# Kernel tuning notes

Measured on AMD Instinct MI355X. Metric: run time of the kernel, lower is better.

The kernel has to match this reference:

```python
import jax, jax.numpy as jnp
import numpy as np

IMG_H, IMG_W = 800, 1216
STRIDE = 16
SIZES = (128.0, 256.0, 512.0)
RATIOS = (0.5, 1.0, 2.0)
NMS_THRESH = 0.7
MIN_SIZE = 16.0
PRE_NMS = 6000   # testing mode
POST_NMS = 300   # testing mode


def _base_anchors():
    # torchvision-style: ratio = h/w, anchors centered at origin, xyxy
    base = []
    for s in SIZES:
        for r in RATIOS:
            hr = np.sqrt(r)
            w, h = s / hr, s * hr
            base.append([-w / 2.0, -h / 2.0, w / 2.0, h / 2.0])
    return jnp.asarray(np.array(base, dtype=np.float32))  # [A,4]


def _anchors(H, W):
    base = _base_anchors()                                  # [A,4]
    sx = jnp.arange(W, dtype=jnp.float32) * STRIDE
    sy = jnp.arange(H, dtype=jnp.float32) * STRIDE
    shift_x, shift_y = jnp.meshgrid(sx, sy)                 # [H,W] each
    shifts = jnp.stack([shift_x, shift_y, shift_x, shift_y], axis=-1)
    # row-major over (h, w), anchors innermost -> matches permute(0,2,3,1) layout
    return (shifts.reshape(-1, 1, 4) + base[None]).reshape(-1, 4)  # [H*W*A,4]


def _conv(x, w, b, pad):
    y = jax.lax.conv_general_dilated(x, w, (1, 1), pad,
                                     dimension_numbers=('NCHW', 'OIHW', 'NCHW'))
    return y + b[None, :, None, None]


def _decode(deltas, anchors):
    wa = anchors[:, 2] - anchors[:, 0]
    ha = anchors[:, 3] - anchors[:, 1]
    cxa = anchors[:, 0] + 0.5 * wa
    cya = anchors[:, 1] + 0.5 * ha
    cx = deltas[:, 0] * wa + cxa
    cy = deltas[:, 1] * ha + cya
    w = jnp.exp(deltas[:, 2]) * wa
    h = jnp.exp(deltas[:, 3]) * ha
    return jnp.stack([cx - 0.5 * w, cy - 0.5 * h, cx + 0.5 * w, cy + 0.5 * h], axis=-1)


def _nms(boxes, scores):
    # boxes: [N,4] sorted by descending score; greedy IoU-suppression NMS
    N = boxes.shape[0]
    areas = (boxes[:, 2] - boxes[:, 0]) * (boxes[:, 3] - boxes[:, 1])

    def body(i, st):
        sup, kidx, kval = st
        avail = jnp.where(sup, -jnp.inf, scores)
        j = jnp.argmax(avail)
        valid = avail[j] > -jnp.inf
        b = boxes[j]
        ix1 = jnp.maximum(b[0], boxes[:, 0])
        iy1 = jnp.maximum(b[1], boxes[:, 1])
        ix2 = jnp.minimum(b[2], boxes[:, 2])
        iy2 = jnp.minimum(b[3], boxes[:, 3])
        inter = jnp.clip(ix2 - ix1, 0.0) * jnp.clip(iy2 - iy1, 0.0)
        union = areas[j] + areas - inter
        iou = jnp.where(union > 0, inter / union, 0.0)
        sup2 = (sup | (iou > NMS_THRESH)).at[j].set(True)
        sup = jnp.where(valid, sup2, sup.at[j].set(True))
        return sup, kidx.at[i].set(j), kval.at[i].set(valid)

    sup0 = jnp.zeros((N,), jnp.bool_)
    _, kidx, kval = jax.lax.fori_loop(
        0, POST_NMS, body,
        (sup0, jnp.zeros((POST_NMS,), jnp.int32), jnp.zeros((POST_NMS,), jnp.bool_)))
    # fixed-size output [POST_NMS,4]; invalid slots zeroed
    return boxes[kidx] * kval[:, None].astype(boxes.dtype)


def setup_inputs() -> dict:
    key = jax.random.key(0)
    ks = jax.random.split(key, 4)
    return {
        'features': jax.random.normal(ks[0], (8, 512, 50, 76), jnp.float32),
        'conv_w': 0.01 * jax.random.normal(ks[1], (512, 512, 3, 3), jnp.float32),
        'conv_b': jnp.zeros((512,), jnp.float32),
        'cls_w': 0.01 * jax.random.normal(ks[2], (9, 512, 1, 1), jnp.float32),
        'cls_b': jnp.zeros((9,), jnp.float32),
        'box_w': 0.01 * jax.random.normal(ks[3], (36, 512, 1, 1), jnp.float32),
        'box_b': jnp.zeros((36,), jnp.float32),
    }


def reference(features, conv_w, conv_b, cls_w, cls_b, box_w, box_b):
    B, _, H, W = features.shape
    t = jax.nn.relu(_conv(features, conv_w, conv_b, 'SAME'))
    obj = _conv(t, cls_w, cls_b, 'VALID')                     # [B,A,H,W]
    objectness = jnp.transpose(obj, (0, 2, 3, 1)).reshape(B, -1)        # [B,N]
    bd = _conv(t, box_w, box_b, 'VALID')                      # [B,4A,H,W]
    bbox_deltas = jnp.transpose(bd, (0, 2, 3, 1)).reshape(B, -1, 4)     # [B,N,4]
    anchors = _anchors(H, W)                                  # [N,4]

    def per_image(scores, deltas):
        props = _decode(deltas, anchors)
        props = jnp.stack([jnp.clip(props[:, 0], 0.0, IMG_W),
                           jnp.clip(props[:, 1], 0.0, IMG_H),
                           jnp.clip(props[:, 2], 0.0, IMG_W),
                           jnp.clip(props[:, 3], 0.0, IMG_H)], axis=-1)
        keep = ((props[:, 2] - props[:, 0]) >= MIN_SIZE) & \
               ((props[:, 3] - props[:, 1]) >= MIN_SIZE)
        s = jnp.where(keep, scores, -jnp.inf)  # small boxes never selected
        top_s, top_i = jax.lax.top_k(s, PRE_NMS)
        return _nms(props[top_i], top_s)

    proposals = jax.vmap(per_image)(objectness, bbox_deltas)  # [B,POST_NMS,4]
    return proposals, objectness, bbox_deltas
```

## Files before the change

kernel.cpp:

```cpp
#include <hip/hip_runtime.h>
#include <stdint.h>
#include <math.h>

typedef unsigned int u32;
typedef unsigned long long u64;
typedef double d4 __attribute__((ext_vector_type(4)));
typedef _Float16 h8 __attribute__((ext_vector_type(8)));
typedef float f32x16 __attribute__((ext_vector_type(16)));

#define NPX    3800
#define NANCH  34200
#define NSEL   6000
#define NOUT   300
#define NPXP   4160

#define OFF_T        0ull
#define OFF_WTH      62259200ull
#define OFF_WTL      66977792ull
#define OFF_BOXES    71696384ull
#define OFF_ITEMS    76073984ull
#define OFF_FSPH     78262784ull
#define OFF_FSPL     112341504ull
#define WS_NEED_F16  146551296ull
#define OFF_PART     OFF_FSPH
#define WS_NEED_SPLITK (OFF_PART + 43776000ull)

#define GLL16(gsrc, ldst) \
    __builtin_amdgcn_global_load_lds((const __attribute__((address_space(1))) void*)(gsrc), \
                                     (__attribute__((address_space(3))) void*)(ldst), 16, 0, 0)

__global__ __launch_bounds__(256) void prep_kernel(const float* __restrict__ feat,
                                                   const float* __restrict__ cw,
                                                   _Float16* __restrict__ wh,
                                                   _Float16* __restrict__ wl,
                                                   _Float16* __restrict__ fh,
                                                   _Float16* __restrict__ fl) {
    const int bid = blockIdx.x;
    const int tid = threadIdx.x;

    if (bid < 9216) {
        int o = bid * 256 + tid;
        int ci = o & 511;
        int co = (o >> 9) & 511;
        int kk = o >> 18;
        float v = cw[(((co << 9) + ci) * 9) + kk] * 1024.0f;
        _Float16 h = (_Float16)v;
        float r = v - (float)h;
        wh[o] = h;
        wl[o] = (_Float16)r;
    } else if (bid < 9216 + 7680) {
        int idx = bid - 9216;
        const int pb = idx % 60; idx /= 60;
        const int b  = idx >> 4;
        const int ci0 = (idx & 15) << 5;
        const int p0  = pb << 6;
        const int px = tid >> 2, cg = tid & 3;
        const int p = p0 + px;
        if (p < NPX) {
            const int yy = p / 76, xx = p - yy * 76;
            h8 vh, vl;
            const float* sp = feat + ((size_t)(b * 512 + ci0 + (cg << 3))) * NPX + p;
            #pragma unroll
            for (int j = 0; j < 8; ++j) {
                float s = sp[(size_t)j * NPX] * 512.0f;
                _Float16 h = (_Float16)s;
                float rr = s - (float)h;
                vh[j] = h;
                vl[j] = (_Float16)rr;
            }
            const size_t dst = ((size_t)b * NPXP + (size_t)((yy + 1) * 80 + xx + 2)) * 512
                             + ci0 + (cg << 3);
            *(h8*)(fh + dst) = vh;
            *(h8*)(fl + dst) = vl;
        }
    } else {
        int idx = (bid - 16896) * 256 + tid;
        int task = idx >> 2, sub = idx & 3;
        if (task < 2880) {
            int b = task / 360, c = task - b * 360;
            int yp, xp;
            if      (c < 80)  { yp = 0;  xp = c; }
            else if (c < 160) { yp = 51; xp = c - 80; }
            else { int c2 = c - 160; yp = 1 + (c2 >> 2); int m = c2 & 3; xp = (m < 2) ? m : (76 + m); }
            const size_t base = ((size_t)b * NPXP + (size_t)(yp * 80 + xp)) * 512 + sub * 128;
            h8 z = {};
            #pragma unroll
            for (int j = 0; j < 16; ++j) {
                *(h8*)(fh + base + (j << 3)) = z;
                *(h8*)(fl + base + (j << 3)) = z;
            }
        }
    }
}

__global__ __launch_bounds__(512, 2) void conv3x3_f16_kernel(
    const _Float16* __restrict__ fh, const _Float16* __restrict__ fl,
    const _Float16* __restrict__ wh, const _Float16* __restrict__ wl,
    const float* __restrict__ bias, float* __restrict__ t)
{
    const int id  = blockIdx.x;
    const int b   = id & 7;
    const int g   = id >> 3;
    const int co0 = (g >> 4) << 7;
    const int pt0 = (g & 15) << 8;
    const int tid = threadIdx.x;
    const int w   = tid >> 6;
    const int l   = tid & 63;
    const int wm  = w >> 2, wn = w & 3;
    const int ln  = l & 31, lk = l >> 5;

    __shared__ __align__(16) _Float16 S[5][24][512];

    const _Float16* sb[3];
    u32 ldof[3];
    bool isA[3];
    const long long fbase = (long long)b * NPXP + pt0;
    #pragma unroll
    for (int i = 0; i < 3; ++i) {
        const int ti = w * 3 + i;
        ldof[i] = (u32)(ti * 1024 + l * 16);
        isA[i] = (ti < 8);
        if (ti < 8) {
            const int mt = ti >> 1, hl = ti & 1;
            sb[i] = (hl ? wl : wh) + ((long long)(co0 + (mt << 5) + ln) << 9) + (lk << 3);
        } else {
            const int tj = ti - 8, nt = tj >> 1, hl = tj & 1;
            sb[i] = (hl ? fl : fh) + ((fbase + (nt << 5) + ln) << 9) + (lk << 3);
        }
    }
    char* lbase = (char*)&S[0][0][0];

    auto stage = [&](int q, int slot) {
        const int kk  = q >> 5;
        const int ci0 = (q & 31) << 4;
        const long long offA = ((long long)kk << 18) + ci0;
        const int kd = (kk * 11) >> 5;
        const int s  = kd * 77 + kk - 81;
        const long long offB = ((long long)s << 9) + ci0;
        char* ld = lbase + slot * 24576;
        #pragma unroll
        for (int i = 0; i < 3; ++i) {
            const long long off = isA[i] ? offA : offB;
            GLL16(sb[i] + off, ld + ldof[i]);
        }
    };

    f32x16 acc[2][2], l2[2][2];
    #pragma unroll
    for (int i = 0; i < 2; ++i)
        #pragma unroll
        for (int j = 0; j < 2; ++j)
            #pragma unroll
            for (int gg = 0; gg < 16; ++gg) { acc[i][j][gg] = 0.0f; l2[i][j][gg] = 0.0f; }

    const int ao = l << 3;

    auto readFrags = [&](int slot, h8* Ah, h8* Al, h8* Bh, h8* Bl) {
        const _Float16* Sq = (const _Float16*)(lbase + slot * 24576);
        #pragma unroll
        for (int i = 0; i < 2; ++i) {
            const int mt = (wm << 1) + i, nt = (wn << 1) + i;
            Ah[i] = *(const h8*)(Sq + (((mt << 1) + 0) << 9) + ao);
            Al[i] = *(const h8*)(Sq + (((mt << 1) + 1) << 9) + ao);
            Bh[i] = *(const h8*)(Sq + ((8 + (nt << 1) + 0) << 9) + ao);
            Bl[i] = *(const h8*)(Sq + ((8 + (nt << 1) + 1) << 9) + ao);
        }
    };

    stage(0, 0); stage(1, 1); stage(2, 2);
    asm volatile("s_waitcnt vmcnt(3)" ::: "memory");
    __builtin_amdgcn_sched_barrier(0);
    __builtin_amdgcn_s_barrier();

    int s0 = 0;
    for (int F = 0; F < 144; ++F) {
        const int q0 = F << 1;
        int s1 = s0 + 1; if (s1 >= 5) s1 -= 5;
        int s3 = s0 + 3; if (s3 >= 5) s3 -= 5;
        int s4 = s0 + 4; if (s4 >= 5) s4 -= 5;
        if (q0 + 3 < 288) stage(q0 + 3, s3);
        if (q0 + 4 < 288) stage(q0 + 4, s4);

        h8 A0h[2], A0l[2], B0h[2], B0l[2];
        h8 A1h[2], A1l[2], B1h[2], B1l[2];
        readFrags(s0, A0h, A0l, B0h, B0l);
        __builtin_amdgcn_s_setprio(1);
        acc[0][0] = __builtin_amdgcn_mfma_f32_32x32x16_f16(A0h[0], B0h[0], acc[0][0], 0, 0, 0);
        acc[0][1] = __builtin_amdgcn_mfma_f32_32x32x16_f16(A0h[0], B0h[1], acc[0][1], 0, 0, 0);
        acc[1][0] = __builtin_amdgcn_mfma_f32_32x32x16_f16(A0h[1], B0h[0], acc[1][0], 0, 0, 0);
        acc[1][1] = __builtin_amdgcn_mfma_f32_32x32x16_f16(A0h[1], B0h[1], acc[1][1], 0, 0, 0);
        acc[0][0] = __builtin_amdgcn_mfma_f32_32x32x16_f16(A0h[0], B0l[0], acc[0][0], 0, 0, 0);
        acc[0][1] = __builtin_amdgcn_mfma_f32_32x32x16_f16(A0h[0], B0l[1], acc[0][1], 0, 0, 0);
        acc[1][0] = __builtin_amdgcn_mfma_f32_32x32x16_f16(A0h[1], B0l[0], acc[1][0], 0, 0, 0);
        acc[1][1] = __builtin_amdgcn_mfma_f32_32x32x16_f16(A0h[1], B0l[1], acc[1][1], 0, 0, 0);
        __builtin_amdgcn_s_setprio(0);
        readFrags(s1, A1h, A1l, B1h, B1l);
        __builtin_amdgcn_s_setprio(1);
        acc[0][0] = __builtin_amdgcn_mfma_f32_32x32x16_f16(A0l[0], B0h[0], acc[0][0], 0, 0, 0);
        acc[0][1] = __builtin_amdgcn_mfma_f32_32x32x16_f16(A0l[0], B0h[1], acc[0][1], 0, 0, 0);
        acc[1][0] = __builtin_amdgcn_mfma_f32_32x32x16_f16(A0l[1], B0h[0], acc[1][0], 0, 0, 0);
        acc[1][1] = __builtin_amdgcn_mfma_f32_32x32x16_f16(A0l[1], B0h[1], acc[1][1], 0, 0, 0);
        acc[0][0] = __builtin_amdgcn_mfma_f32_32x32x16_f16(A1h[0], B1h[0], acc[0][0], 0, 0, 0);
        acc[0][1] = __builtin_amdgcn_mfma_f32_32x32x16_f16(A1h[0], B1h[1], acc[0][1], 0, 0, 0);
        acc[1][0] = __builtin_amdgcn_mfma_f32_32x32x16_f16(A1h[1], B1h[0], acc[1][0], 0, 0, 0);
        acc[1][1] = __builtin_amdgcn_mfma_f32_32x32x16_f16(A1h[1], B1h[1], acc[1][1], 0, 0, 0);
        acc[0][0] = __builtin_amdgcn_mfma_f32_32x32x16_f16(A1h[0], B1l[0], acc[0][0], 0, 0, 0);
        acc[0][1] = __builtin_amdgcn_mfma_f32_32x32x16_f16(A1h[0], B1l[1], acc[0][1], 0, 0, 0);
        acc[1][0] = __builtin_amdgcn_mfma_f32_32x32x16_f16(A1h[1], B1l[0], acc[1][0], 0, 0, 0);
        acc[1][1] = __builtin_amdgcn_mfma_f32_32x32x16_f16(A1h[1], B1l[1], acc[1][1], 0, 0, 0);
        acc[0][0] = __builtin_amdgcn_mfma_f32_32x32x16_f16(A1l[0], B1h[0], acc[0][0], 0, 0, 0);
        acc[0][1] = __builtin_amdgcn_mfma_f32_32x32x16_f16(A1l[0], B1h[1], acc[0][1], 0, 0, 0);
        acc[1][0] = __builtin_amdgcn_mfma_f32_32x32x16_f16(A1l[1], B1h[0], acc[1][0], 0, 0, 0);
        acc[1][1] = __builtin_amdgcn_mfma_f32_32x32x16_f16(A1l[1], B1h[1], acc[1][1], 0, 0, 0);
        __builtin_amdgcn_s_setprio(0);

        if (((q0 + 1) & 7) == 7) {
            #pragma unroll
            for (int i = 0; i < 2; ++i)
                #pragma unroll
                for (int j = 0; j < 2; ++j) {
                    l2[i][j] += acc[i][j];
                    #pragma unroll
                    for (int gg = 0; gg < 16; ++gg) acc[i][j][gg] = 0.0f;
                }
        }

        if (F < 143) {
            if (q0 + 4 < 288) { asm volatile("s_waitcnt vmcnt(3)" ::: "memory"); }
            else              { asm volatile("s_waitcnt vmcnt(0)" ::: "memory"); }
            __builtin_amdgcn_sched_barrier(0);
            __builtin_amdgcn_s_barrier();
        }
        s0 += 2; if (s0 >= 5) s0 -= 5;
    }

    int rcp[16];
    {
        h8 pa, pb;
        #pragma unroll
        for (int j = 0; j < 8; ++j) { pa[j] = (_Float16)(float)ln; pb[j] = (_Float16)0.0625f; }
        f32x16 pr, pc;
        #pragma unroll
        for (int gg = 0; gg < 16; ++gg) { pr[gg] = 0.0f; pc[gg] = 0.0f; }
        pr = __builtin_amdgcn_mfma_f32_32x32x16_f16(pa, pb, pr, 0, 0, 0);
        pc = __builtin_amdgcn_mfma_f32_32x32x16_f16(pb, pa, pc, 0, 0, 0);
        #pragma unroll
        for (int gg = 0; gg < 16; ++gg)
            rcp[gg] = ((int)(pr[gg] + 0.5f)) | (((int)(pc[gg] + 0.5f)) << 8);
    }

    const double dsc = 1.0 / 524288.0;
    #pragma unroll
    for (int i = 0; i < 2; ++i) {
        #pragma unroll
        for (int j = 0; j < 2; ++j) {
            #pragma unroll
            for (int gg = 0; gg < 16; ++gg) {
                const int row = rcp[gg] & 255;
                const int col = rcp[gg] >> 8;
                const int co  = co0 + (wm << 6) + (i << 5) + row;
                const int pp  = pt0 + (wn << 6) + (j << 5) + col;
                const int yy  = pp / 80;
                const int xx  = pp - yy * 80;
                if (yy >= 1 && yy < 51 && xx >= 2 && xx < 78) {
                    const double v = (double)l2[i][j][gg] * dsc + (double)bias[co];
                    t[((size_t)(b * 512 + co)) * NPX + (yy - 1) * 76 + (xx - 2)]
                        = (float)(v > 0.0 ? v : 0.0);
                }
            }
        }
    }
}

__global__ __launch_bounds__(1024) void wtrans_kernel(const float* __restrict__ cw,
                                                      float* __restrict__ wt) {
    int o = blockIdx.x * 1024 + threadIdx.x;
    if (o >= 512*512*9) return;
    int co = o & 511;
    int ci = (o >> 9) & 511;
    int kk = o >> 18;
    wt[o] = cw[((co << 9) + ci) * 9 + kk];
}

__global__ __launch_bounds__(256, 2) void conv3x3_mfma_kernel(const float* __restrict__ feat,
                                                              const float* __restrict__ wt,
                                                              const float* __restrict__ bias,
                                                              float* __restrict__ t) {
    const int b   = blockIdx.z;
    const int co0 = blockIdx.y << 7;
    const int px0 = blockIdx.x << 6;
    const int tid = threadIdx.x;
    const int w    = tid >> 6;
    const int l    = tid & 63;
    const int quad = l >> 4;
    const int lc   = l & 15;

    __shared__ double BsF[2][1024];

    int rr[4], cc[4];
    {
        d4 pzr = {0.0, 0.0, 0.0, 0.0};
        d4 pzc = {0.0, 0.0, 0.0, 0.0};
        double paM = (double)lc;
        double pbN = (double)lc;
        pzr = __builtin_amdgcn_mfma_f64_16x16x4f64(paM, 1.0, pzr, 0, 0, 0);
        pzc = __builtin_amdgcn_mfma_f64_16x16x4f64(1.0, pbN, pzc, 0, 0, 0);
        #pragma unroll
        for (int g = 0; g < 4; ++g) {
            rr[g] = (((int)pzr[g]) >> 2) & 15;
            cc[g] = (((int)pzc[g]) >> 2) & 15;
        }
    }

    d4 acc[2][4];
    #pragma unroll
    for (int i = 0; i < 2; ++i)
        #pragma unroll
        for (int j = 0; j < 4; ++j) acc[i][j] = (d4){0.0, 0.0, 0.0, 0.0};

    const float* featb = feat + (size_t)b * 512 * NPX;

    const int b_quad = (tid >> 4) & 3;
    const int b_pxl  = ((tid >> 6) << 4) | (tid & 15);
    const int p      = px0 + b_pxl;
    const int py     = p / 76;
    const int px     = p - py * 76;
    const bool pvalid = (p < NPX);

    float vaf[8], vbf[4];
    double a_cur[8];

    auto loadA = [&](int q, float* va) {
        int kk  = q >> 5;
        int ci0 = (q & 31) << 4;
        const float* ap = wt + (((size_t)(kk * 512 + ci0 + quad)) << 9)
                             + co0 + (w << 5) + lc;
        #pragma unroll
        for (int ks = 0; ks < 4; ++ks) {
            va[ks * 2 + 0] = ap[(ks << 11)];
            va[ks * 2 + 1] = ap[(ks << 11) + 16];
        }
    };
    auto loadB = [&](int q, float* vb) {
        int kk  = q >> 5;
        int ci0 = (q & 31) << 4;
        int kd = kk / 3;
        int dy = kd - 1, dx = kk - kd * 3 - 1;
        int iy = py + dy, ix = px + dx;
        bool ok = pvalid && ((unsigned)iy < 50u) && ((unsigned)ix < 76u);
        if (ok) {
            const float* bp = featb + (size_t)(ci0 + b_quad) * NPX + iy * 76 + ix;
            #pragma unroll
            for (int j = 0; j < 4; ++j) vb[j] = bp[(size_t)(j << 2) * NPX];
        } else {
            vb[0] = vb[1] = vb[2] = vb[3] = 0.0f;
        }
    };

    loadA(0, vaf); loadB(0, vbf);
    #pragma unroll
    for (int j = 0; j < 4; ++j) BsF[0][tid + (j << 8)] = (double)vbf[j];
    #pragma unroll
    for (int j = 0; j < 8; ++j) a_cur[j] = (double)vaf[j];
    __syncthreads();

    for (int q = 0; q < 288; ++q) {
        const int cur = q & 1;
        if (q < 287) { loadA(q + 1, vaf); loadB(q + 1, vbf); }
        const double* bb = BsF[cur];
        #pragma unroll
        for (int ks = 0; ks < 4; ++ks) {
            const double* bp = bb + (ks << 8);
            double a0 = a_cur[ks * 2], a1 = a_cur[ks * 2 + 1];
            #pragma unroll
            for (int nt = 0; nt < 4; ++nt) {
                double bv = bp[(nt << 6) + l];
                acc[0][nt] = __builtin_amdgcn_mfma_f64_16x16x4f64(a0, bv, acc[0][nt], 0, 0, 0);
                acc[1][nt] = __builtin_amdgcn_mfma_f64_16x16x4f64(a1, bv, acc[1][nt], 0, 0, 0);
            }
        }
        if (q < 287) {
            #pragma unroll
            for (int j = 0; j < 4; ++j) BsF[cur ^ 1][tid + (j << 8)] = (double)vbf[j];
            #pragma unroll
            for (int j = 0; j < 8; ++j) a_cur[j] = (double)vaf[j];
            __syncthreads();
        }
    }

    #pragma unroll
    for (int mt = 0; mt < 2; ++mt) {
        #pragma unroll
        for (int g = 0; g < 4; ++g) {
            int co = co0 + (w << 5) + (mt << 4) + rr[g];
            double bs = (double)bias[co];
            float* row = t + ((size_t)b * 512 + co) * NPX;
            #pragma unroll
            for (int nt = 0; nt < 4; ++nt) {
                int pp = px0 + (nt << 4) + cc[g];
                if (pp < NPX) {
                    double v = acc[mt][nt][g] + bs;
                    row[pp] = (float)(v > 0.0 ? v : 0.0);
                }
            }
        }
    }
}

__global__ __launch_bounds__(64) void heads_partial_kernel(const float* __restrict__ t,
                                                           const float* __restrict__ cls_w,
                                                           const float* __restrict__ box_w,
                                                           double* __restrict__ part) {
    const int b = blockIdx.y, c = blockIdx.z;
    const int p = blockIdx.x * 64 + threadIdx.x;
    if (p >= NPX) return;
    const float* tb = t + ((size_t)b * 512 + c * 128) * NPX + p;

    double ac[9]  = {};
    double ab[36] = {};
    for (int ci = 0; ci < 128; ++ci) {
        double tv = (double)tb[(size_t)ci * NPX];
        int cw = c * 128 + ci;
        #pragma unroll
        for (int o = 0; o < 9;  ++o) ac[o] = fma((double)cls_w[o * 512 + cw], tv, ac[o]);
        #pragma unroll
        for (int o = 0; o < 36; ++o) ab[o] = fma((double)box_w[o * 512 + cw], tv, ab[o]);
    }
    double* dst = part + ((size_t)(c * 8 + b) * 45) * NPX + p;
    #pragma unroll
    for (int o = 0; o < 9;  ++o) dst[(size_t)o * NPX] = ac[o];
    #pragma unroll
    for (int o = 0; o < 36; ++o) dst[(size_t)(9 + o) * NPX] = ab[o];
}

__device__ __forceinline__ void decode_px(int b, int p, const double* s45,
                                          const float* cls_b, const float* box_b,
                                          float* out_obj, float* out_del,
                                          float* boxes, u64* items) {
    float* ob = out_obj + (size_t)b * NANCH + (size_t)p * 9;
    float* dl = out_del + (size_t)b * NANCH * 4 + (size_t)p * 36;
    const int yy = p / 76, xx = p - yy * 76;

    #pragma unroll
    for (int a = 0; a < 9; ++a) {
        double s  = s45[a] + (double)cls_b[a];
        ob[a] = (float)s;
        double d0 = s45[9 + 4*a + 0] + (double)box_b[4*a+0];
        double d1 = s45[9 + 4*a + 1] + (double)box_b[4*a+1];
        double d2 = s45[9 + 4*a + 2] + (double)box_b[4*a+2];
        double d3 = s45[9 + 4*a + 3] + (double)box_b[4*a+3];
        dl[4*a+0] = (float)d0; dl[4*a+1] = (float)d1;
        dl[4*a+2] = (float)d2; dl[4*a+3] = (float)d3;

        int si = a / 3, ri = a - si * 3;
        double sz = (si == 0) ? 128.0 : ((si == 1) ? 256.0 : 512.0);
        double hr = (ri == 0) ? 0.7071067811865476 : ((ri == 1) ? 1.0 : 1.4142135623730951);
        float bx2f = (float)(sz / hr * 0.5);
        float by2f = (float)(sz * hr * 0.5);

        double sx = (double)(xx * 16), sy = (double)(yy * 16);
        double x1 = sx - (double)bx2f, x2 = sx + (double)bx2f;
        double y1 = sy - (double)by2f, y2 = sy + (double)by2f;

        double wa = x2 - x1, ha = y2 - y1;
        double cxa = x1 + 0.5 * wa, cya = y1 + 0.5 * ha;
        double cx = d0 * wa + cxa, cy = d1 * ha + cya;
        double w  = exp(d2) * wa,  h  = exp(d3) * ha;

        double px1 = cx - 0.5 * w, py1 = cy - 0.5 * h;
        double px2 = cx + 0.5 * w, py2 = cy + 0.5 * h;
        px1 = fmin(fmax(px1, 0.0), 1216.0);
        py1 = fmin(fmax(py1, 0.0), 800.0);
        px2 = fmin(fmax(px2, 0.0), 1216.0);
        py2 = fmin(fmax(py2, 0.0), 800.0);

        bool keep = ((px2 - px1) >= 16.0) && ((py2 - py1) >= 16.0);
        double se = keep ? s : -INFINITY;

        u64 ubits = (u64)__double_as_longlong(se);
        u64 ka = (ubits >> 63) ? ~ubits : (ubits | 0x8000000000000000ull);
        u64 kd = ~ka;
        int n = p * 9 + a;
        items[(size_t)b * NANCH + n] = (kd & ~0xFFFFull) | (u64)(u32)n;
        *(float4*)(boxes + ((size_t)b * NANCH + n) * 4) =
            make_float4((float)px1, (float)py1, (float)px2, (float)py2);
    }
}

__global__ __launch_bounds__(64) void reduce_decode_kernel(const double* __restrict__ part,
                                                           const float* __restrict__ cls_b,
                                                           const float* __restrict__ box_b,
                                                           float* __restrict__ out_obj,
                                                           float* __restrict__ out_del,
                                                           float* __restrict__ boxes,
                                                           u64* __restrict__ items) {
    const int b = blockIdx.y;
    const int p = blockIdx.x * 64 + threadIdx.x;
    if (p >= NPX) return;
    double s45[45];
    #pragma unroll
    for (int o = 0; o < 45; ++o) {
        double s = part[((size_t)(0 * 8 + b) * 45 + o) * NPX + p];
        s += part[((size_t)(1 * 8 + b) * 45 + o) * NPX + p];
        s += part[((size_t)(2 * 8 + b) * 45 + o) * NPX + p];
        s += part[((size_t)(3 * 8 + b) * 45 + o) * NPX + p];
        s45[o] = s;
    }
    decode_px(b, p, s45, cls_b, box_b, out_obj, out_del, boxes, items);
}

__global__ __launch_bounds__(256) void heads_decode_kernel(const float* __restrict__ t,
                                                           const float* __restrict__ cls_w,
                                                           const float* __restrict__ cls_b,
                                                           const float* __restrict__ box_w,
                                                           const float* __restrict__ box_b,
                                                           float* __restrict__ out_obj,
                                                           float* __restrict__ out_del,
                                                           float* __restrict__ boxes,
                                                           u64* __restrict__ items) {
    const int b = blockIdx.y;
    const int p = blockIdx.x * 256 + threadIdx.x;
    if (p >= NPX) return;
    const float* tb = t + (size_t)b * 512 * NPX + p;
    double s45[45];
    #pragma unroll
    for (int o = 0; o < 45; ++o) s45[o] = 0.0;
    for (int ci = 0; ci < 512; ++ci) {
        double tv = (double)tb[(size_t)ci * NPX];
        #pragma unroll
        for (int o = 0; o < 9;  ++o) s45[o]     = fma((double)cls_w[o * 512 + ci], tv, s45[o]);
        #pragma unroll
        for (int o = 0; o < 36; ++o) s45[9 + o] = fma((double)box_w[o * 512 + ci], tv, s45[9 + o]);
    }
    decode_px(b, p, s45, cls_b, box_b, out_obj, out_del, boxes, items);
}

__device__ __forceinline__ bool iou_gt(float4 A, float4 B, float areaA, float areaB) {
    float ix1 = fmaxf(A.x, B.x), iy1 = fmaxf(A.y, B.y);
    float ix2 = fminf(A.z, B.z), iy2 = fminf(A.w, B.w);
    float iw = fmaxf(ix2 - ix1, 0.0f), ih = fmaxf(iy2 - iy1, 0.0f);
    float inter = iw * ih;
    float uni = areaA + areaB - inter;
    float iou = (uni > 0.0f) ? (inter / uni) : 0.0f;
    return iou > 0.7f;
}

__global__ __launch_bounds__(1024) void topk_nms_kernel(const u64* __restrict__ items,
                                                        const float* __restrict__ boxes,
                                                        float* __restrict__ out) {
    extern __shared__ u64 buf[];
    u32* hist = (u32*)buf;
    u32* scan = hist + 4096;
    u32* scal = hist + 5120;

    const int b   = blockIdx.x;
    const int tid = threadIdx.x;
    const u64* it = items + (size_t)b * NANCH;

    #pragma unroll
    for (int i = 0; i < 4; ++i) hist[tid * 4 + i] = 0;
    __syncthreads();
    for (int i = tid; i < NANCH; i += 1024)
        atomicAdd(&hist[(u32)(it[i] >> 52)], 1);
    __syncthreads();

    u32 B1, cum1;
    {
        u32 c0 = hist[tid*4], c1 = hist[tid*4+1], c2 = hist[tid*4+2], c3 = hist[tid*4+3];
        u32 S = c0 + c1 + c2 + c3;
        scan[tid] = S;
        __syncthreads();
        for (int off = 1; off < 1024; off <<= 1) {
            u32 v = (tid >= off) ? scan[tid - off] : 0;
            __syncthreads();
            scan[tid] += v;
            __syncthreads();
        }
        u32 excl = scan[tid] - S;
        const u32 target = 5999;
        if (target >= excl && target < excl + S) {
            u32 pfx = excl, bidx, cum;
            if      (target < pfx + c0)           { bidx = tid*4;   cum = pfx; }
            else if (target < pfx + c0 + c1)      { bidx = tid*4+1; cum = pfx + c0; }
            else if (target < pfx + c0 + c1 + c2) { bidx = tid*4+2; cum = pfx + c0 + c1; }
            else                                  { bidx = tid*4+3; cum = pfx + c0 + c1 + c2; }
            scal[0] = bidx; scal[1] = cum;
        }
    }
    __syncthreads();
    B1 = scal[0]; cum1 = scal[1];
    __syncthreads();

    #pragma unroll
    for (int i = 0; i < 4; ++i) hist[tid * 4 + i] = 0;
    __syncthreads();
    for (int i = tid; i < NANCH; i += 1024) {
        u64 v = it[i];
        if ((u32)(v >> 52) == B1)
            atomicAdd(&hist[(u32)(v >> 40) & 0xFFF], 1);
    }
    __syncthreads();

    u32 B2;
    {
        u32 c0 = hist[tid*4], c1 = hist[tid*4+1], c2 = hist[tid*4+2], c3 = hist[tid*4+3];
        u32 S = c0 + c1 + c2 + c3;
        scan[tid] = S;
        __syncthreads();
        for (int off = 1; off < 1024; off <<= 1) {
            u32 v = (tid >= off) ? scan[tid - off] : 0;
            __syncthreads();
            scan[tid] += v;
            __syncthreads();
        }
        u32 excl = scan[tid] - S;
        const u32 target = 5999 - cum1;
        if (target >= excl && target < excl + S) {
            u32 pfx = excl, bidx;
            if      (target < pfx + c0)           bidx = tid*4;
            else if (target < pfx + c0 + c1)      bidx = tid*4+1;
            else if (target < pfx + c0 + c1 + c2) bidx = tid*4+2;
            else                                  bidx = tid*4+3;
            scal[2] = bidx;
        }
    }
    __syncthreads();
    B2 = scal[2];
    const u32 T = ((B1 << 12) | B2) + 1;
    __syncthreads();

    for (int i = tid; i < 8192; i += 1024) buf[i] = ~0ull;
    __syncthreads();
    u32* cnt = (u32*)&buf[8191];
    if (tid == 0) *cnt = 0;
    __syncthreads();
    for (int i = tid; i < NANCH; i += 1024) {
        u64 v = it[i];
        if ((u32)(v >> 40) < T) {
            u32 pos = atomicAdd(cnt, 1);
            if (pos < 8191) buf[pos] = v;
        }
    }
    __syncthreads();
    if (tid == 0) buf[8191] = ~0ull;
    __syncthreads();

    for (int size = 2; size <= 8192; size <<= 1) {
        for (int stride = size >> 1; stride > 0; stride >>= 1) {
            #pragma unroll
            for (int v = 0; v < 4; ++v) {
                int idx = tid + (v << 10);
                int i = 2 * idx - (idx & (stride - 1));
                int j = i + stride;
                bool up = ((i & size) == 0);
                u64 x = buf[i], y = buf[j];
                if ((x > y) == up) { buf[i] = y; buf[j] = x; }
            }
            __syncthreads();
        }
    }

    float4 bx6[6]; u32 dead6[6];
    #pragma unroll
    for (int s = 0; s < 6; ++s) {
        int r = tid + (s << 10);
        u64 v = buf[r];
        bool dd = (r >= NSEL) || ((u32)(v >> 32) >= 0xFFF00000u);
        float4 bb = make_float4(0.f, 0.f, 0.f, 0.f);
        if (!dd) {
            u32 n = (u32)(v & 0xFFFFull);
            bb = *(const float4*)(boxes + ((size_t)b * NANCH + n) * 4);
        }
        bx6[s] = bb;
        dead6[s] = dd ? 1u : 0u;
    }
    __syncthreads();

    float4* candbox = (float4*)buf;
    u64*    wmask   = (u64*)(buf + 2560);
    float4* accb    = (float4*)(buf + 3072);
    u32*    cntp    = (u32*)(buf + 3712);
    if (tid == 0) *cntp = 0;
    __syncthreads();

    for (int s = 0; s < 6; ++s) {
        int count = (int)*cntp;
        if (count >= NOUT) break;
        float4 mb = bx6[s];
        float  ma = (mb.z - mb.x) * (mb.w - mb.y);
        bool dd = dead6[s] != 0;
        for (int a2 = 0; a2 < count && !dd; ++a2) {
            float4 abx = accb[a2];
            if (iou_gt(mb, abx, ma, (abx.z - abx.x) * (abx.w - abx.y))) dd = true;
        }
        candbox[tid] = mb;
        u64 bal = __ballot(!dd);
        if ((tid & 63) == 0) wmask[tid >> 6] = bal;
        __syncthreads();
        if (tid < 64) {
            int cnt2 = count;
            for (int w2 = 0; w2 < 16 && cnt2 < NOUT; ++w2) {
                u64 mm = wmask[w2];
                while (mm != 0 && cnt2 < NOUT) {
                    int bit = __ffsll(mm) - 1;
                    mm &= (mm - 1);
                    float4 cb = candbox[(w2 << 6) + bit];
                    float  ca = (cb.z - cb.x) * (cb.w - cb.y);
                    bool okc = true;
                    for (int base = count; base < cnt2 && okc; base += 64) {
                        int idx = base + tid;
                        bool bad = false;
                        if (idx < cnt2) {
                            float4 abx = accb[idx];
                            bad = iou_gt(cb, abx, ca, (abx.z - abx.x) * (abx.w - abx.y));
                        }
                        if (__any(bad)) okc = false;
                    }
                    if (okc) {
                        if (tid == 0) accb[cnt2] = cb;
                        cnt2++;
                    }
                }
            }
            if (tid == 0) *cntp = (u32)cnt2;
        }
        __syncthreads();
    }

    int fin = (int)*cntp;
    for (int r = tid; r < NOUT; r += 1024) {
        float4 v = (r < fin) ? accb[r] : make_float4(0.f, 0.f, 0.f, 0.f);
        *(float4*)(out + ((size_t)b * NOUT + r) * 4) = v;
    }
}

extern "C" void kernel_launch(void* const* d_in, const int* in_sizes, int n_in,
                              void* d_out, int out_size, void* d_ws, size_t ws_size,
                              hipStream_t stream) {
    const float* feat   = (const float*)d_in[0];
    const float* conv_w = (const float*)d_in[1];
    const float* conv_b = (const float*)d_in[2];
    const float* cls_w  = (const float*)d_in[3];
    const float* cls_b  = (const float*)d_in[4];
    const float* box_w  = (const float*)d_in[5];
    const float* box_b  = (const float*)d_in[6];

    float* out       = (float*)d_out;
    float* out_props = out;
    float* out_obj   = out + 9600;
    float* out_del   = out + 9600 + 273600;

    char* ws = (char*)d_ws;
    float*    t     = (float*)(ws + OFF_T);
    _Float16* wth   = (_Float16*)(ws + OFF_WTH);
    _Float16* wtl   = (_Float16*)(ws + OFF_WTL);
    float*    wtf   = (float*)(ws + OFF_WTH);
    float*    boxes = (float*)(ws + OFF_BOXES);
    u64*      items = (u64*)(ws + OFF_ITEMS);
    _Float16* fsph  = (_Float16*)(ws + OFF_FSPH);
    _Float16* fspl  = (_Float16*)(ws + OFF_FSPL);
    double*   part  = (double*)(ws + OFF_PART);

    if (ws_size >= WS_NEED_F16) {
        hipLaunchKernelGGL(prep_kernel, dim3(16941), dim3(256), 0, stream,
                           feat, conv_w, wth, wtl, fsph, fspl);
        hipLaunchKernelGGL(conv3x3_f16_kernel, dim3(512), dim3(512), 0, stream,
                           fsph, fspl, wth, wtl, conv_b, t);
    } else {
        hipLaunchKernelGGL(wtrans_kernel, dim3(2304), dim3(1024), 0, stream, conv_w, wtf);
        hipLaunchKernelGGL(conv3x3_mfma_kernel, dim3(60, 4, 8), dim3(256), 0, stream,
                           feat, wtf, conv_b, t);
    }
    if (ws_size >= WS_NEED_SPLITK) {
        hipLaunchKernelGGL(heads_partial_kernel, dim3(60, 8, 4), dim3(64), 0, stream,
                           t, cls_w, box_w, part);
        hipLaunchKernelGGL(reduce_decode_kernel, dim3(60, 8), dim3(64), 0, stream,
                           part, cls_b, box_b, out_obj, out_del, boxes, items);
    } else {
        hipLaunchKernelGGL(heads_decode_kernel, dim3(15, 8), dim3(256), 0, stream,
                           t, cls_w, cls_b, box_w, box_b, out_obj, out_del, boxes, items);
    }
    hipLaunchKernelGGL(topk_nms_kernel, dim3(8), dim3(1024), 65536, stream,
                       items, boxes, out_props);
}
```

Baseline: 1.103 ms.

## Fuse split-K heads and reduce-decode into one kernel with LDS reduction

Replaces the two-kernel split-K head path, which wrote double partial sums to global memory and then reduced them, with a single kernel. Each block of four 32-thread groups computes the four channel-slices and reduces them through shared memory before decoding. The weight conversion in prep is also restructured so each thread reads nine contiguous taps at once instead of doing strided gathers, which shrinks the prep grid. This saves a launch and the global round-trip for the partials, at the cost of blocks of 128 threads in which only 32 threads run the decode.

New measurement: 1.172 ms. +6.3%, slower.

```diff
diff --git a/kernel.cpp b/kernel.cpp
--- a/kernel.cpp
+++ b/kernel.cpp
@@ -22,8 +22,6 @@
 #define OFF_FSPH     78262784ull
 #define OFF_FSPL     112341504ull
 #define WS_NEED_F16  146551296ull
-#define OFF_PART     OFF_FSPH
-#define WS_NEED_SPLITK (OFF_PART + 43776000ull)
 
 #define GLL16(gsrc, ldst) \
     __builtin_amdgcn_global_load_lds((const __attribute__((address_space(1))) void*)(gsrc), \
@@ -38,18 +36,22 @@
     const int bid = blockIdx.x;
     const int tid = threadIdx.x;
 
-    if (bid < 9216) {
-        int o = bid * 256 + tid;
-        int ci = o & 511;
-        int co = (o >> 9) & 511;
-        int kk = o >> 18;
-        float v = cw[(((co << 9) + ci) * 9) + kk] * 1024.0f;
-        _Float16 h = (_Float16)v;
-        float r = v - (float)h;
-        wh[o] = h;
-        wl[o] = (_Float16)r;
-    } else if (bid < 9216 + 7680) {
-        int idx = bid - 9216;
+    if (bid < 1024) {
+        const int o = bid * 256 + tid;
+        const float* src = cw + (size_t)o * 9;
+        float v[9];
+        #pragma unroll
+        for (int k = 0; k < 9; ++k) v[k] = src[k];
+        #pragma unroll
+        for (int kk = 0; kk < 9; ++kk) {
+            float s = v[kk] * 1024.0f;
+            _Float16 h = (_Float16)s;
+            float r = s - (float)h;
+            wh[((size_t)kk << 18) + o] = h;
+            wl[((size_t)kk << 18) + o] = (_Float16)r;
+        }
+    } else if (bid < 1024 + 7680) {
+        int idx = bid - 1024;
         const int pb = idx % 60; idx /= 60;
         const int b  = idx >> 4;
         const int ci0 = (idx & 15) << 5;
@@ -74,7 +76,7 @@
             *(h8*)(fl + dst) = vl;
         }
     } else {
-        int idx = (bid - 16896) * 256 + tid;
+        int idx = (bid - 8704) * 256 + tid;
         int task = idx >> 2, sub = idx & 3;
         if (task < 2880) {
             int b = task / 360, c = task - b * 360;
@@ -407,32 +409,6 @@
     }
 }
 
-__global__ __launch_bounds__(64) void heads_partial_kernel(const float* __restrict__ t,
-                                                           const float* __restrict__ cls_w,
-                                                           const float* __restrict__ box_w,
-                                                           double* __restrict__ part) {
-    const int b = blockIdx.y, c = blockIdx.z;
-    const int p = blockIdx.x * 64 + threadIdx.x;
-    if (p >= NPX) return;
-    const float* tb = t + ((size_t)b * 512 + c * 128) * NPX + p;
-
-    double ac[9]  = {};
-    double ab[36] = {};
-    for (int ci = 0; ci < 128; ++ci) {
-        double tv = (double)tb[(size_t)ci * NPX];
-        int cw = c * 128 + ci;
-        #pragma unroll
-        for (int o = 0; o < 9;  ++o) ac[o] = fma((double)cls_w[o * 512 + cw], tv, ac[o]);
-        #pragma unroll
-        for (int o = 0; o < 36; ++o) ab[o] = fma((double)box_w[o * 512 + cw], tv, ab[o]);
-    }
-    double* dst = part + ((size_t)(c * 8 + b) * 45) * NPX + p;
-    #pragma unroll
-    for (int o = 0; o < 9;  ++o) dst[(size_t)o * NPX] = ac[o];
-    #pragma unroll
-    for (int o = 0; o < 36; ++o) dst[(size_t)(9 + o) * NPX] = ab[o];
-}
-
 __device__ __forceinline__ void decode_px(int b, int p, const double* s45,
                                           const float* cls_b, const float* box_b,
                                           float* out_obj, float* out_del,
@@ -487,26 +463,53 @@
     }
 }
 
-__global__ __launch_bounds__(64) void reduce_decode_kernel(const double* __restrict__ part,
-                                                           const float* __restrict__ cls_b,
-                                                           const float* __restrict__ box_b,
-                                                           float* __restrict__ out_obj,
-                                                           float* __restrict__ out_del,
-                                                           float* __restrict__ boxes,
-                                                           u64* __restrict__ items) {
-    const int b = blockIdx.y;
-    const int p = blockIdx.x * 64 + threadIdx.x;
-    if (p >= NPX) return;
-    double s45[45];
-    #pragma unroll
-    for (int o = 0; o < 45; ++o) {
-        double s = part[((size_t)(0 * 8 + b) * 45 + o) * NPX + p];
-        s += part[((size_t)(1 * 8 + b) * 45 + o) * NPX + p];
-        s += part[((size_t)(2 * 8 + b) * 45 + o) * NPX + p];
-        s += part[((size_t)(3 * 8 + b) * 45 + o) * NPX + p];
-        s45[o] = s;
-    }
-    decode_px(b, p, s45, cls_b, box_b, out_obj, out_del, boxes, items);
+__global__ __launch_bounds__(128) void heads_fused_kernel(const float* __restrict__ t,
+                                                          const float* __restrict__ cls_w,
+                                                          const float* __restrict__ cls_b,
+                                                          const float* __restrict__ box_w,
+                                                          const float* __restrict__ box_b,
+                                                          float* __restrict__ out_obj,
+                                                          float* __restrict__ out_del,
+                                                          float* __restrict__ boxes,
+                                                          u64* __restrict__ items) {
+    __shared__ double s45p[4][45][32];
+    const int b  = blockIdx.y;
+    const int tid = threadIdx.x;
+    const int c  = tid >> 5;
+    const int pl = tid & 31;
+    const int p  = blockIdx.x * 32 + pl;
+
+    double ac[9]  = {};
+    double ab[36] = {};
+    if (p < NPX) {
+        const float* tb = t + ((size_t)b * 512 + c * 128) * NPX + p;
+        for (int ci = 0; ci < 128; ++ci) {
+            double tv = (double)tb[(size_t)ci * NPX];
+            int cw = c * 128 + ci;
+            #pragma unroll
+            for (int o = 0; o < 9;  ++o) ac[o] = fma((double)cls_w[o * 512 + cw], tv, ac[o]);
+            #pragma unroll
+            for (int o = 0; o < 36; ++o) ab[o] = fma((double)box_w[o * 512 + cw], tv, ab[o]);
+        }
+    }
+    #pragma unroll
+    for (int o = 0; o < 9;  ++o) s45p[c][o][pl] = ac[o];
+    #pragma unroll
+    for (int o = 0; o < 36; ++o) s45p[c][9 + o][pl] = ab[o];
+    __syncthreads();
+
+    if (tid < 32 && p < NPX) {
+        double s45[45];
+        #pragma unroll
+        for (int o = 0; o < 45; ++o) {
+            double s = s45p[0][o][pl];
+            s += s45p[1][o][pl];
+            s += s45p[2][o][pl];
+            s += s45p[3][o][pl];
+            s45[o] = s;
+        }
+        decode_px(b, p, s45, cls_b, box_b, out_obj, out_del, boxes, items);
+    }
 }
 
 __global__ __launch_bounds__(256) void heads_decode_kernel(const float* __restrict__ t,
@@ -759,24 +762,18 @@
     u64*      items = (u64*)(ws + OFF_ITEMS);
     _Float16* fsph  = (_Float16*)(ws + OFF_FSPH);
     _Float16* fspl  = (_Float16*)(ws + OFF_FSPL);
-    double*   part  = (double*)(ws + OFF_PART);
 
     if (ws_size >= WS_NEED_F16) {
-        hipLaunchKernelGGL(prep_kernel, dim3(16941), dim3(256), 0, stream,
+        hipLaunchKernelGGL(prep_kernel, dim3(8749), dim3(256), 0, stream,
                            feat, conv_w, wth, wtl, fsph, fspl);
         hipLaunchKernelGGL(conv3x3_f16_kernel, dim3(512), dim3(512), 0, stream,
                            fsph, fspl, wth, wtl, conv_b, t);
+        hipLaunchKernelGGL(heads_fused_kernel, dim3(119, 8), dim3(128), 0, stream,
+                           t, cls_w, cls_b, box_w, box_b, out_obj, out_del, boxes, items);
     } else {
         hipLaunchKernelGGL(wtrans_kernel, dim3(2304), dim3(1024), 0, stream, conv_w, wtf);
         hipLaunchKernelGGL(conv3x3_mfma_kernel, dim3(60, 4, 8), dim3(256), 0, stream,
                            feat, wtf, conv_b, t);
-    }
-    if (ws_size >= WS_NEED_SPLITK) {
-        hipLaunchKernelGGL(heads_partial_kernel, dim3(60, 8, 4), dim3(64), 0, stream,
-                           t, cls_w, box_w, part);
-        hipLaunchKernelGGL(reduce_decode_kernel, dim3(60, 8), dim3(64), 0, stream,
-                           part, cls_b, box_b, out_obj, out_del, boxes, items);
-    } else {
         hipLaunchKernelGGL(heads_decode_kernel, dim3(15, 8), dim3(256), 0, stream,
                            t, cls_w, cls_b, box_w, box_b, out_obj, out_del, boxes, items);
     }
```
